# Kernel tuning notes

Hardware: AMD Instinct MI355X
Metric: run time of the kernel (lower is better)

The kernel has to match this reference:

```python
import jax, jax.numpy as jnp
import numpy as np

B, C, H, W = 4, 256, 48, 48
KD, NH, AR = 32, 8, 4
D = AR * KD            # 128, value dim per head
NHKD = NH * KD         # 256
DH = NH * D            # 1024
EPS = 1e-5


def _bn(y, g, b):
    # BN with fresh running stats (mean=0, var=1): y*g/sqrt(1+eps)+b, over channel dim
    s = g / jnp.sqrt(jnp.float32(1.0) + EPS)
    return y * s[None, :, None] + b[None, :, None]


def setup_inputs() -> dict:
    key = jax.random.key(0)
    ks = jax.random.split(key, 13)
    w = lambda k, sh: jax.random.normal(k, sh, jnp.float32) * 0.05
    g = lambda k, sh: 1.0 + jax.random.normal(k, sh, jnp.float32) * 0.05
    return {
        "x": jax.random.normal(ks[0], (B, C, H, W), jnp.float32),
        "wq": w(ks[1], (NHKD, C)), "gq": g(ks[2], (NHKD,)), "bq": w(ks[3], (NHKD,)),
        "wk": w(ks[4], (NHKD, C)), "gk": g(ks[5], (NHKD,)), "bk": w(ks[6], (NHKD,)),
        "wv": w(ks[7], (DH, C)),   "gv": g(ks[8], (DH,)),   "bv": w(ks[9], (DH,)),
        "wp": w(ks[10], (C, DH)),  "gp": g(ks[11], (C,)),   "bp": w(ks[12], (C,)),
    }


def reference(x, wq, gq, bq, wk, gk, bk, wv, gv, bv, wp, gp, bp):
    b, c, h, w = x.shape
    n = h * w
    xf = x.reshape(b, c, n)                                   # [B,C,N]
    # 1x1 conv == channel matmul, then BN
    q = _bn(jnp.einsum('oc,bcn->bon', wq, xf), gq, bq).reshape(b, NH, KD, n)
    k = _bn(jnp.einsum('oc,bcn->bon', wk, xf), gk, bk).reshape(b, NH, KD, n)
    v = _bn(jnp.einsum('oc,bcn->bon', wv, xf), gv, bv).reshape(b, NH, D, n)
    # NOTE: original forward does NOT apply self.scale
    attn = jax.nn.softmax(jnp.einsum('bhkn,bhkm->bhnm', q, k), axis=-1)  # [B,H,N,N]
    xx = jnp.einsum('bhnm,bhdm->bhdn', attn, v).reshape(b, DH, n)        # [B,DH,N]
    out = _bn(jnp.einsum('oc,bcn->bon', wp, jax.nn.relu(xx)), gp, bp)
    return out.reshape(b, c, h, w)
```

## Files before the change

### kernel.cpp

```cpp
#include <hip/hip_runtime.h>

#define BB 4
#define C 256
#define HW 2304
#define NH 8
#define KD 32
#define D 128
#define DH 1024
#define MQ 256

typedef unsigned short bf16u;
typedef __attribute__((ext_vector_type(8))) short short8;
typedef __attribute__((ext_vector_type(4))) short bfx4;
typedef __attribute__((ext_vector_type(4))) float f32x4;
typedef __attribute__((ext_vector_type(4))) unsigned ux4;
typedef __attribute__((ext_vector_type(2))) unsigned ux2;

union U8 { ux4 u; short8 s; };
union V8 { short8 s; bfx4 h[2]; };

__device__ __forceinline__ bf16u f2b(float f) {
    unsigned u = __float_as_uint(f);
    return (bf16u)((u + 0x7fffu + ((u >> 16) & 1u)) >> 16);
}
__device__ __forceinline__ unsigned pkb(float a, float b) {
    return __builtin_amdgcn_perm(__float_as_uint(b) + 0x8000u,
                                 __float_as_uint(a) + 0x8000u, 0x07060302u);
}

__device__ __forceinline__ void glds16(const bf16u* g, bf16u* l) {
    __builtin_amdgcn_global_load_lds(
        (const __attribute__((address_space(1))) unsigned int*)g,
        (__attribute__((address_space(3))) unsigned int*)l,
        16, 0, 0);
}

#define MFMA32 __builtin_amdgcn_mfma_f32_16x16x32_bf16

__global__ __launch_bounds__(256) void prep(
    const float* __restrict__ wq, const float* __restrict__ wk, const float* __restrict__ wv,
    const float* __restrict__ gq, const float* __restrict__ bq,
    const float* __restrict__ gk, const float* __restrict__ bk,
    const float* __restrict__ gv, const float* __restrict__ bv,
    bf16u* __restrict__ Wc, float* __restrict__ biasc)
{
    const float rs = rsqrtf(1.0f + 1e-5f);
    const float L2E = 1.4426950408889634f;
    const int t = threadIdx.x, blk = blockIdx.x;
    if (blk < 192) {
        const int idx = (blk*256 + t) * 8;
        const int row = idx >> 8;
        const float* src; float sc;
        if (idx < 65536)       { src = wq + idx;            sc = gq[row]*rs*L2E; }
        else if (idx < 131072) { src = wk + (idx - 65536);  sc = gk[row-256]*rs; }
        else                   { src = wv + (idx - 131072); sc = gv[row-512]*rs; }
        float4 a = *(const float4*)(src);
        float4 c = *(const float4*)(src + 4);
        ux4 v;
        v.x = pkb(a.x*sc, a.y*sc); v.y = pkb(a.z*sc, a.w*sc);
        v.z = pkb(c.x*sc, c.y*sc); v.w = pkb(c.z*sc, c.w*sc);
        *(ux4*)(Wc + idx) = v;
    } else {
        #pragma unroll
        for (int k = 0; k < 6; ++k) {
            const int r = k*256 + t;
            float v;
            if (r < 256)      v = bq[r] * L2E;
            else if (r < 512) v = bk[r - 256];
            else              v = bv[r - 512];
            biasc[r] = v;
        }
    }
}

__global__ __launch_bounds__(256) void xtrans(const float* __restrict__ x,
                                              bf16u* __restrict__ xT)
{
    const int c0 = blockIdx.x * 64, n0 = blockIdx.y * 64, b = blockIdx.z;
    const int t = threadIdx.x;
    __shared__ float tile[64][68];

    const float* xb = x + (size_t)b * C * HW;
    #pragma unroll
    for (int rr = 0; rr < 4; ++rr) {
        const int cl = rr*16 + (t >> 4);
        float4 v = *(const float4*)(xb + (size_t)(c0 + cl) * HW + n0 + (t & 15)*4);
        tile[cl][(t&15)*4+0] = v.x; tile[cl][(t&15)*4+1] = v.y;
        tile[cl][(t&15)*4+2] = v.z; tile[cl][(t&15)*4+3] = v.w;
    }
    __syncthreads();
    const int nl = t >> 2, ch = t & 3;
    short8 v0, v1;
    #pragma unroll
    for (int kk = 0; kk < 8; ++kk) v0[kk] = (short)f2b(tile[ch*16+kk][nl]);
    #pragma unroll
    for (int kk = 0; kk < 8; ++kk) v1[kk] = (short)f2b(tile[ch*16+8+kk][nl]);
    bf16u* dst = xT + ((size_t)b*HW + n0 + nl) * C + c0 + ch*16;
    *(short8*)(dst)     = v0;
    *(short8*)(dst + 8) = v1;
}

__global__ __launch_bounds__(256, 3) void qkv_gemm(
    const bf16u* __restrict__ Wc, const float* __restrict__ biasc,
    const bf16u* __restrict__ xT,
    bf16u* __restrict__ qT, bf16u* __restrict__ kT, bf16u* __restrict__ vO)
{
    const int mt = blockIdx.x, ntb = blockIdx.y, b = blockIdx.z;
    const int r0 = mt * 128, c0 = ntb * 128;
    const int t = threadIdx.x, w = t >> 6, l = t & 63;
    const int l15 = l & 15, q = l >> 4;
    const int wr = w >> 1, wc = w & 1;

    __shared__ bf16u smem[24576];

    const bf16u* xb = xT + (size_t)b * HW * C;

    const int sA0 = (w*2+0)*64 + l, sA1 = (w*2+1)*64 + l;
    const bf16u* gA0 = Wc + (size_t)(r0 + (sA0>>2)) * C + (sA0&3)*8;
    const bf16u* gA1 = Wc + (size_t)(r0 + (sA1>>2)) * C + (sA1&3)*8;
    const bf16u* gB0 = xb + (size_t)(c0 + (sA0>>2)) * C + (sA0&3)*8;
    const bf16u* gB1 = xb + (size_t)(c0 + (sA1>>2)) * C + (sA1&3)*8;

    f32x4 acc[4][4];
    #pragma unroll
    for (int i = 0; i < 4; ++i)
        #pragma unroll
        for (int j = 0; j < 4; ++j) { acc[i][j][0]=0.f; acc[i][j][1]=0.f; acc[i][j][2]=0.f; acc[i][j][3]=0.f; }

    auto stage = [&](int it2, int bb) {
        const int k0 = it2 * 32;
        bf16u* As = smem + bb*4096;
        bf16u* Bs = smem + 12288 + bb*4096;
        glds16(gA0 + k0, As + (w*2+0)*512);
        glds16(gA1 + k0, As + (w*2+1)*512);
        glds16(gB0 + k0, Bs + (w*2+0)*512);
        glds16(gB1 + k0, Bs + (w*2+1)*512);
    };

    const bool isV = (r0 >= 512);
    stage(0, 0); stage(1, 1);
    for (int it = 0; it < 8; ++it) {
        __syncthreads();
        if (it + 2 < 8) stage(it + 2, (it + 2) % 3);
        const bf16u* A = smem + (it % 3) * 4096;
        const bf16u* B = smem + 12288 + (it % 3) * 4096;
        short8 af[4], bf[4];
        #pragma unroll
        for (int i = 0; i < 4; ++i) af[i] = *(const short8*)(A + (wr*64 + i*16 + l15)*32 + q*8);
        #pragma unroll
        for (int j = 0; j < 4; ++j) bf[j] = *(const short8*)(B + (wc*64 + j*16 + l15)*32 + q*8);
        if (!isV) {
            #pragma unroll
            for (int i = 0; i < 4; ++i)
                #pragma unroll
                for (int j = 0; j < 4; ++j)
                    acc[i][j] = MFMA32(af[i], bf[j], acc[i][j], 0, 0, 0);
        } else {
            #pragma unroll
            for (int i = 0; i < 4; ++i)
                #pragma unroll
                for (int j = 0; j < 4; ++j)
                    acc[i][j] = MFMA32(bf[j], af[i], acc[i][j], 0, 0, 0);
        }
    }

    __syncthreads();
    bf16u* Od = smem + w * 4096;

    if (!isV) {
        float bC[4][4];
        #pragma unroll
        for (int i = 0; i < 4; ++i)
            #pragma unroll
            for (int r = 0; r < 4; ++r)
                bC[i][r] = biasc[r0 + wr*64 + i*16 + q*4 + r];
        #pragma unroll
        for (int i = 0; i < 4; ++i)
            #pragma unroll
            for (int j = 0; j < 4; ++j) {
                float y0 = acc[i][j][0] + bC[i][0];
                float y1 = acc[i][j][1] + bC[i][1];
                float y2 = acc[i][j][2] + bC[i][2];
                float y3 = acc[i][j][3] + bC[i][3];
                ux2 pk; pk.x = pkb(y0, y1); pk.y = pkb(y2, y3);
                const int row = j*16 + l15;
                const int ch  = (i*2 + (q >> 1)) ^ (l15 & 7);
                *(ux2*)(Od + row*64 + ch*8 + (q & 1)*4) = pk;
            }
        bf16u* dst = (r0 < 256) ? qT : kT;
        const int n = c0 + wc*64 + l;
        #pragma unroll
        for (int c = 0; c < 8; ++c) {
            short8 v = *(const short8*)(Od + l*64 + ((c ^ (l & 7)) * 8));
            const int ocg = (r0 & 255) + wr*64 + c*8;
            const int h = ocg >> 5, kd0 = ocg & 31;
            *(short8*)(dst + ((size_t)(b*NH + h) * HW + n) * KD + kd0) = v;
        }
    } else {
        float bC[4];
        #pragma unroll
        for (int i = 0; i < 4; ++i)
            bC[i] = biasc[r0 + wr*64 + i*16 + l15];
        #pragma unroll
        for (int i = 0; i < 4; ++i)
            #pragma unroll
            for (int j = 0; j < 4; ++j) {
                float y0 = acc[i][j][0] + bC[i];
                float y1 = acc[i][j][1] + bC[i];
                float y2 = acc[i][j][2] + bC[i];
                float y3 = acc[i][j][3] + bC[i];
                ux2 pk; pk.x = pkb(y0, y1); pk.y = pkb(y2, y3);
                const int row = i*16 + l15;
                const int ch  = (j*2 + (q >> 1)) ^ (l15 & 7);
                *(ux2*)(Od + row*64 + ch*8 + (q & 1)*4) = pk;
            }
        bf16u* dst = vO + (size_t)b * DH * HW;
        const int d = (r0 - 512) + wr*64 + l;
        #pragma unroll
        for (int c = 0; c < 8; ++c) {
            short8 v = *(const short8*)(Od + l*64 + ((c ^ (l & 7)) * 8));
            const int n = c0 + wc*64 + c*8;
            *(short8*)(dst + (size_t)d * HW + n) = v;
        }
    }
}

__global__ __launch_bounds__(256, 3) void attn_mfma(
    const bf16u* __restrict__ qT, const bf16u* __restrict__ kT,
    const bf16u* __restrict__ vg, bf16u* __restrict__ xg)
{
    const int nt = blockIdx.x, h = blockIdx.y, b = blockIdx.z;
    const int n0 = nt * 128;
    const int t = threadIdx.x;
    const int w = t >> 6, l = t & 63, l15 = l & 15, q = l >> 4;

    const bf16u* qTh = qT + (size_t)(b*NH + h) * HW * KD;
    const bf16u* kTh = kT + (size_t)(b*NH + h) * HW * KD;
    const bf16u* vh  = vg + ((size_t)b*DH + (size_t)h*D) * HW;

    __shared__ bf16u smem[20480];

    short8 qf0 = *(const short8*)(qTh + (size_t)(n0 + w*32 +      l15) * KD + q*8);
    short8 qf1 = *(const short8*)(qTh + (size_t)(n0 + w*32 + 16 + l15) * KD + q*8);

    f32x4 o[2][8];
    #pragma unroll
    for (int a = 0; a < 2; ++a)
        #pragma unroll
        for (int d = 0; d < 8; ++d) { o[a][d][0]=0.f; o[a][d][1]=0.f; o[a][d][2]=0.f; o[a][d][3]=0.f; }
    float psum0 = 0.f, psum1 = 0.f;
    const f32x4 zero = {0.f, 0.f, 0.f, 0.f};

    auto stage = [&](int m0, int bb) {
        bf16u* Ks = smem + bb*2048;
        bf16u* Vs = smem + 4096 + bb*8192;
        glds16(kTh + (size_t)m0*KD + (w*64 + l)*8, Ks + w*512);
        #pragma unroll
        for (int j = 0; j < 4; ++j) {
            const int s = (w*4 + j)*64 + l;
            const int d = s >> 3, c = s & 7, cg = c ^ (d & 7);
            glds16(vh + (size_t)d*HW + m0 + cg*8, Vs + (w*4 + j)*512);
        }
    };

    stage(0, 0);
    for (int mt = 0; mt < 36; ++mt) {
        __syncthreads();
        if (mt < 35) stage((mt+1)*64, (mt+1)&1);
        const bf16u* Ks = smem + (mt&1)*2048;
        const bf16u* Vs = smem + 4096 + (mt&1)*8192;

        f32x4 st0[4], st1[4];
        #pragma unroll
        for (int kt = 0; kt < 4; ++kt) {
            short8 kf = *(const short8*)(Ks + (kt*16 + l15)*KD + q*8);
            st0[kt] = MFMA32(kf, qf0, zero, 0, 0, 0);
            st1[kt] = MFMA32(kf, qf1, zero, 0, 0, 0);
        }

        unsigned dA0[4], dB0[4], dA1[4], dB1[4];
        #pragma unroll
        for (int kt = 0; kt < 4; ++kt) {
            float p0 = __builtin_amdgcn_exp2f(st0[kt][0]);
            float p1 = __builtin_amdgcn_exp2f(st0[kt][1]);
            float p2 = __builtin_amdgcn_exp2f(st0[kt][2]);
            float p3 = __builtin_amdgcn_exp2f(st0[kt][3]);
            psum0 += (p0 + p1) + (p2 + p3);
            dA0[kt] = pkb(p0, p1); dB0[kt] = pkb(p2, p3);
            float r0_ = __builtin_amdgcn_exp2f(st1[kt][0]);
            float r1_ = __builtin_amdgcn_exp2f(st1[kt][1]);
            float r2_ = __builtin_amdgcn_exp2f(st1[kt][2]);
            float r3_ = __builtin_amdgcn_exp2f(st1[kt][3]);
            psum1 += (r0_ + r1_) + (r2_ + r3_);
            dA1[kt] = pkb(r0_, r1_); dB1[kt] = pkb(r2_, r3_);
        }

        #pragma unroll
        for (int kh = 0; kh < 2; ++kh) {
            U8 u0, u1;
            u0.u[0] = dA0[kh*2];   u0.u[1] = dB0[kh*2];
            u0.u[2] = dA0[kh*2+1]; u0.u[3] = dB0[kh*2+1];
            u1.u[0] = dA1[kh*2];   u1.u[1] = dB1[kh*2];
            u1.u[2] = dA1[kh*2+1]; u1.u[3] = dB1[kh*2+1];
            const int clo = kh*4 + (q >> 1);
            const int chi = clo + 2;
            const int sub = (q & 1) * 4;
            #pragma unroll
            for (int dt = 0; dt < 8; ++dt) {
                const int d = dt*16 + l15;
                V8 vv;
                vv.h[0] = *(const bfx4*)(Vs + d*64 + ((clo ^ (d & 7)) * 8) + sub);
                vv.h[1] = *(const bfx4*)(Vs + d*64 + ((chi ^ (d & 7)) * 8) + sub);
                o[0][dt] = MFMA32(u0.s, vv.s, o[0][dt], 0, 0, 0);
                o[1][dt] = MFMA32(u1.s, vv.s, o[1][dt], 0, 0, 0);
            }
        }
    }

    psum0 += __shfl_xor(psum0, 16); psum0 += __shfl_xor(psum0, 32);
    psum1 += __shfl_xor(psum1, 16); psum1 += __shfl_xor(psum1, 32);
    float inv0[4], inv1[4];
    #pragma unroll
    for (int r = 0; r < 4; ++r) {
        inv0[r] = 1.0f / __shfl(psum0, q*4 + r);
        inv1[r] = 1.0f / __shfl(psum1, q*4 + r);
    }
    __syncthreads();
    bf16u* Od = smem + w * 4352;
    #pragma unroll
    for (int dt = 0; dt < 8; ++dt)
        #pragma unroll
        for (int r = 0; r < 4; ++r) {
            float v0 = fmaxf(o[0][dt][r] * inv0[r], 0.f);
            float v1 = fmaxf(o[1][dt][r] * inv1[r], 0.f);
            Od[(     q*4 + r)*136 + dt*16 + l15] = f2b(v0);
            Od[(16 + q*4 + r)*136 + dt*16 + l15] = f2b(v1);
        }
    bf16u* xb = xg + ((size_t)b*HW + n0 + w*32) * DH + h*D;
    #pragma unroll
    for (int rr = 0; rr < 2; ++rr) {
        const int row = rr*16 + (l >> 2), c = l & 3;
        #pragma unroll
        for (int kk = 0; kk < 4; ++kk)
            *(short8*)(xb + (size_t)row*DH + c*32 + kk*8) =
                *(const short8*)(Od + row*136 + c*32 + kk*8);
    }
}

__global__ __launch_bounds__(256, 3) void out_gemm(
    const float* __restrict__ wp, const float* __restrict__ gp, const float* __restrict__ bp,
    const bf16u* __restrict__ xx, float* __restrict__ out)
{
    const int mt = blockIdx.x, ntb = blockIdx.y, b = blockIdx.z;
    const int r0 = mt * 64, c0 = ntb * 64;
    const int t = threadIdx.x, w = t >> 6, l = t & 63;
    const int l15 = l & 15, q = l >> 4;
    const int wr = w >> 1, wc = w & 1;

    __shared__ bf16u smem[24576];

    const bf16u* xb = xx + (size_t)b * HW * DH;

    const int sA0 = t, sA1 = 256 + t;
    const float* gA0 = wp + (size_t)(r0 + (sA0>>3)) * DH + (sA0&7)*8;
    const float* gA1 = wp + (size_t)(r0 + (sA1>>3)) * DH + (sA1&7)*8;
    const int sB0 = w*128 + l, sB1 = w*128 + 64 + l;
    const bf16u* gB0 = xb + (size_t)(c0 + (sB0>>3)) * DH + (sB0&7)*8;
    const bf16u* gB1 = xb + (size_t)(c0 + (sB1>>3)) * DH + (sB1&7)*8;

    f32x4 acc[2][2];
    #pragma unroll
    for (int i = 0; i < 2; ++i)
        #pragma unroll
        for (int j = 0; j < 2; ++j) { acc[i][j][0]=0.f; acc[i][j][1]=0.f; acc[i][j][2]=0.f; acc[i][j][3]=0.f; }

    auto stage = [&](int it2, int bb) {
        const int k0 = it2 * 64;
        bf16u* As = smem + bb*4096;
        bf16u* Bs = smem + 12288 + bb*4096;
        glds16(gB0 + k0, Bs + (w*2+0)*512);
        glds16(gB1 + k0, Bs + (w*2+1)*512);
        #pragma unroll
        for (int jj = 0; jj < 2; ++jj) {
            const float* ga = jj ? gA1 : gA0;
            const int    s  = jj ? sA1 : sA0;
            float4 a = *(const float4*)(ga + k0);
            float4 c = *(const float4*)(ga + k0 + 4);
            ux4 v;
            v.x = pkb(a.x, a.y); v.y = pkb(a.z, a.w);
            v.z = pkb(c.x, c.y); v.w = pkb(c.z, c.w);
            *(ux4*)(As + s*8) = v;
        }
    };

    stage(0, 0); stage(1, 1);
    for (int it = 0; it < 16; ++it) {
        __syncthreads();
        if (it + 2 < 16) stage(it + 2, (it + 2) % 3);
        const bf16u* A = smem + (it % 3) * 4096;
        const bf16u* B = smem + 12288 + (it % 3) * 4096;
        #pragma unroll
        for (int kk = 0; kk < 2; ++kk) {
            short8 af[2], bf[2];
            #pragma unroll
            for (int i = 0; i < 2; ++i) af[i] = *(const short8*)(A + (wr*32 + i*16 + l15)*64 + kk*32 + q*8);
            #pragma unroll
            for (int j = 0; j < 2; ++j) bf[j] = *(const short8*)(B + (wc*32 + j*16 + l15)*64 + kk*32 + q*8);
            #pragma unroll
            for (int i = 0; i < 2; ++i)
                #pragma unroll
                for (int j = 0; j < 2; ++j)
                    acc[i][j] = MFMA32(af[i], bf[j], acc[i][j], 0, 0, 0);
        }
    }

    const float rs = rsqrtf(1.0f + 1e-5f);
    #pragma unroll
    for (int i = 0; i < 2; ++i)
        #pragma unroll
        for (int r = 0; r < 4; ++r) {
            const int oc = r0 + wr*32 + i*16 + q*4 + r;
            const float s = gp[oc]*rs, bi = bp[oc];
            #pragma unroll
            for (int j = 0; j < 2; ++j) {
                const int n = c0 + wc*32 + j*16 + l15;
                out[((size_t)b*C + oc)*HW + n] = acc[i][j][r]*s + bi;
            }
        }
}

extern "C" void kernel_launch(void* const* d_in, const int* in_sizes, int n_in,
                              void* d_out, int out_size, void* d_ws, size_t ws_size,
                              hipStream_t stream) {
    const float* x  = (const float*)d_in[0];
    const float* wq = (const float*)d_in[1];
    const float* gq = (const float*)d_in[2];
    const float* bq = (const float*)d_in[3];
    const float* wk = (const float*)d_in[4];
    const float* gk = (const float*)d_in[5];
    const float* bk = (const float*)d_in[6];
    const float* wv = (const float*)d_in[7];
    const float* gv = (const float*)d_in[8];
    const float* bv = (const float*)d_in[9];
    const float* wp = (const float*)d_in[10];
    const float* gp = (const float*)d_in[11];
    const float* bp = (const float*)d_in[12];
    float* out = (float*)d_out;

    bf16u* qw = (bf16u*)d_ws;
    bf16u* kw = qw + (size_t)BB * MQ * HW;
    bf16u* vw = kw + (size_t)BB * MQ * HW;
    bf16u* xw = vw + (size_t)BB * DH * HW;
    bf16u* xTb = xw;
    bf16u* Wc  = xw + (size_t)BB * MQ * HW;
    float* biasc = (float*)(Wc + 393216);

    hipLaunchKernelGGL(prep, dim3(193), dim3(256), 0, stream,
                       wq, wk, wv, gq, bq, gk, bk, gv, bv, Wc, biasc);
    hipLaunchKernelGGL(xtrans, dim3(4, 36, BB), dim3(256), 0, stream, x, xTb);
    hipLaunchKernelGGL(qkv_gemm, dim3(12, 18, BB), dim3(256), 0, stream,
                       Wc, biasc, xTb, qw, kw, vw);
    hipLaunchKernelGGL(attn_mfma, dim3(18, NH, BB), dim3(256), 0, stream,
                       qw, kw, vw, xw);
    hipLaunchKernelGGL(out_gemm, dim3(4, 36, BB), dim3(256), 0, stream,
                       wp, gp, bp, xw, out);
}
```

Measured before the change: 213.7 us.

## Pre-tile weights for direct LDS loads, permute V layout, shrink attention tiles

Weights for the QKV and output GEMMs are pre-converted into a tiled bf16 layout, so the GEMMs stage A with global_load_lds and no per-iteration fp32 conversion. The output projection's BN scale is folded into the weights by a new prep2 kernel. V is stored in a permuted order so attention reads full 16-byte V fragments. Attention now uses 64-row query tiles with K fragments held in registers and prefetched, doubling the grid and raising occupancy. The cost is an extra launch and heavier register/global traffic for K.

New measurement: 219.5 us. 2.7% more time.

```diff
diff --git a/kernel.cpp b/kernel.cpp
--- a/kernel.cpp
+++ b/kernel.cpp
@@ -42,7 +42,7 @@
     const float* __restrict__ gq, const float* __restrict__ bq,
     const float* __restrict__ gk, const float* __restrict__ bk,
     const float* __restrict__ gv, const float* __restrict__ bv,
-    bf16u* __restrict__ Wc, float* __restrict__ biasc)
+    bf16u* __restrict__ WcT, float* __restrict__ biasc)
 {
     const float rs = rsqrtf(1.0f + 1e-5f);
     const float L2E = 1.4426950408889634f;
@@ -50,20 +50,23 @@
     if (blk < 192) {
         const int idx = (blk*256 + t) * 8;
         const int row = idx >> 8;
+        const int k   = idx & 255;
         const float* src; float sc;
-        if (idx < 65536)       { src = wq + idx;            sc = gq[row]*rs*L2E; }
-        else if (idx < 131072) { src = wk + (idx - 65536);  sc = gk[row-256]*rs; }
-        else                   { src = wv + (idx - 131072); sc = gv[row-512]*rs; }
+        if (row < 256)      { src = wq + idx;            sc = gq[row]*rs*L2E; }
+        else if (row < 512) { src = wk + (idx - 65536);  sc = gk[row-256]*rs; }
+        else                { src = wv + (idx - 131072); sc = gv[row-512]*rs; }
         float4 a = *(const float4*)(src);
         float4 c = *(const float4*)(src + 4);
         ux4 v;
         v.x = pkb(a.x*sc, a.y*sc); v.y = pkb(a.z*sc, a.w*sc);
         v.z = pkb(c.x*sc, c.y*sc); v.w = pkb(c.z*sc, c.w*sc);
-        *(ux4*)(Wc + idx) = v;
+        const size_t dst = (size_t)((row>>7)*8 + (k>>5))*4096
+                         + (size_t)((row&127)*4 + ((k&31)>>3))*8;
+        *(ux4*)(WcT + dst) = v;
     } else {
         #pragma unroll
-        for (int k = 0; k < 6; ++k) {
-            const int r = k*256 + t;
+        for (int kk = 0; kk < 6; ++kk) {
+            const int r = kk*256 + t;
             float v;
             if (r < 256)      v = bq[r] * L2E;
             else if (r < 512) v = bk[r - 256];
@@ -101,7 +104,7 @@
 }
 
 __global__ __launch_bounds__(256, 3) void qkv_gemm(
-    const bf16u* __restrict__ Wc, const float* __restrict__ biasc,
+    const bf16u* __restrict__ WcT, const float* __restrict__ biasc,
     const bf16u* __restrict__ xT,
     bf16u* __restrict__ qT, bf16u* __restrict__ kT, bf16u* __restrict__ vO)
 {
@@ -115,9 +118,9 @@
 
     const bf16u* xb = xT + (size_t)b * HW * C;
 
-    const int sA0 = (w*2+0)*64 + l, sA1 = (w*2+1)*64 + l;
-    const bf16u* gA0 = Wc + (size_t)(r0 + (sA0>>2)) * C + (sA0&3)*8;
-    const bf16u* gA1 = Wc + (size_t)(r0 + (sA1>>2)) * C + (sA1&3)*8;
+    const int sA0 = w*128 + l, sA1 = w*128 + 64 + l;
+    const bf16u* gA0 = WcT + (size_t)mt*32768 + (size_t)sA0*8;
+    const bf16u* gA1 = WcT + (size_t)mt*32768 + (size_t)sA1*8;
     const bf16u* gB0 = xb + (size_t)(c0 + (sA0>>2)) * C + (sA0&3)*8;
     const bf16u* gB1 = xb + (size_t)(c0 + (sA1>>2)) * C + (sA1&3)*8;
 
@@ -128,13 +131,12 @@
         for (int j = 0; j < 4; ++j) { acc[i][j][0]=0.f; acc[i][j][1]=0.f; acc[i][j][2]=0.f; acc[i][j][3]=0.f; }
 
     auto stage = [&](int it2, int bb) {
-        const int k0 = it2 * 32;
         bf16u* As = smem + bb*4096;
         bf16u* Bs = smem + 12288 + bb*4096;
-        glds16(gA0 + k0, As + (w*2+0)*512);
-        glds16(gA1 + k0, As + (w*2+1)*512);
-        glds16(gB0 + k0, Bs + (w*2+0)*512);
-        glds16(gB1 + k0, Bs + (w*2+1)*512);
+        glds16(gA0 + it2*4096, As + sA0*8);
+        glds16(gA1 + it2*4096, As + sA1*8);
+        glds16(gB0 + it2*32,   Bs + sA0*8);
+        glds16(gB1 + it2*32,   Bs + sA1*8);
     };
 
     const bool isV = (r0 >= 512);
@@ -218,19 +220,25 @@
         const int d = (r0 - 512) + wr*64 + l;
         #pragma unroll
         for (int c = 0; c < 8; ++c) {
-            short8 v = *(const short8*)(Od + l*64 + ((c ^ (l & 7)) * 8));
-            const int n = c0 + wc*64 + c*8;
-            *(short8*)(dst + (size_t)d * HW + n) = v;
-        }
-    }
-}
-
-__global__ __launch_bounds__(256, 3) void attn_mfma(
+            V8 v; v.s = *(const short8*)(Od + l*64 + ((c ^ (l & 7)) * 8));
+            const int kh = c >> 2;
+            const int g0 = (2*c) & 7;
+            const int pos0 = kh*32 + (g0 & 3)*8 + (g0 >> 2)*4;
+            const int g1 = g0 + 1;
+            const int pos1 = kh*32 + (g1 & 3)*8 + (g1 >> 2)*4;
+            bf16u* dr = dst + (size_t)d * HW + c0 + wc*64;
+            *(bfx4*)(dr + pos0) = v.h[0];
+            *(bfx4*)(dr + pos1) = v.h[1];
+        }
+    }
+}
+
+__global__ __launch_bounds__(256, 4) void attn_mfma(
     const bf16u* __restrict__ qT, const bf16u* __restrict__ kT,
     const bf16u* __restrict__ vg, bf16u* __restrict__ xg)
 {
     const int nt = blockIdx.x, h = blockIdx.y, b = blockIdx.z;
-    const int n0 = nt * 128;
+    const int n0 = nt * 64;
     const int t = threadIdx.x;
     const int w = t >> 6, l = t & 63, l15 = l & 15, q = l >> 4;
 
@@ -238,23 +246,18 @@
     const bf16u* kTh = kT + (size_t)(b*NH + h) * HW * KD;
     const bf16u* vh  = vg + ((size_t)b*DH + (size_t)h*D) * HW;
 
-    __shared__ bf16u smem[20480];
-
-    short8 qf0 = *(const short8*)(qTh + (size_t)(n0 + w*32 +      l15) * KD + q*8);
-    short8 qf1 = *(const short8*)(qTh + (size_t)(n0 + w*32 + 16 + l15) * KD + q*8);
-
-    f32x4 o[2][8];
-    #pragma unroll
-    for (int a = 0; a < 2; ++a)
-        #pragma unroll
-        for (int d = 0; d < 8; ++d) { o[a][d][0]=0.f; o[a][d][1]=0.f; o[a][d][2]=0.f; o[a][d][3]=0.f; }
-    float psum0 = 0.f, psum1 = 0.f;
+    __shared__ bf16u smem[16384];
+
+    short8 qf = *(const short8*)(qTh + (size_t)(n0 + w*16 + l15) * KD + q*8);
+
+    f32x4 o[8];
+    #pragma unroll
+    for (int d = 0; d < 8; ++d) { o[d][0]=0.f; o[d][1]=0.f; o[d][2]=0.f; o[d][3]=0.f; }
+    float psum = 0.f;
     const f32x4 zero = {0.f, 0.f, 0.f, 0.f};
 
-    auto stage = [&](int m0, int bb) {
-        bf16u* Ks = smem + bb*2048;
-        bf16u* Vs = smem + 4096 + bb*8192;
-        glds16(kTh + (size_t)m0*KD + (w*64 + l)*8, Ks + w*512);
+    auto stageV = [&](int m0, int bb) {
+        bf16u* Vs = smem + bb*8192;
         #pragma unroll
         for (int j = 0; j < 4; ++j) {
             const int s = (w*4 + j)*64 + l;
@@ -263,92 +266,103 @@
         }
     };
 
-    stage(0, 0);
+    short8 kfc[4];
+    #pragma unroll
+    for (int kt = 0; kt < 4; ++kt)
+        kfc[kt] = *(const short8*)(kTh + (size_t)(kt*16 + l15) * KD + q*8);
+    stageV(0, 0);
+
     for (int mt = 0; mt < 36; ++mt) {
         __syncthreads();
-        if (mt < 35) stage((mt+1)*64, (mt+1)&1);
-        const bf16u* Ks = smem + (mt&1)*2048;
-        const bf16u* Vs = smem + 4096 + (mt&1)*8192;
-
-        f32x4 st0[4], st1[4];
+        if (mt < 35) stageV((mt+1)*64, (mt+1)&1);
+        const bf16u* Vs = smem + (mt&1)*8192;
+
+        short8 kfn[4];
+        if (mt < 35) {
+            #pragma unroll
+            for (int kt = 0; kt < 4; ++kt)
+                kfn[kt] = *(const short8*)(kTh + (size_t)((mt+1)*64 + kt*16 + l15) * KD + q*8);
+        }
+
+        f32x4 st[4];
+        #pragma unroll
+        for (int kt = 0; kt < 4; ++kt)
+            st[kt] = MFMA32(kfc[kt], qf, zero, 0, 0, 0);
+
+        unsigned dA[4], dB[4];
         #pragma unroll
         for (int kt = 0; kt < 4; ++kt) {
-            short8 kf = *(const short8*)(Ks + (kt*16 + l15)*KD + q*8);
-            st0[kt] = MFMA32(kf, qf0, zero, 0, 0, 0);
-            st1[kt] = MFMA32(kf, qf1, zero, 0, 0, 0);
-        }
-
-        unsigned dA0[4], dB0[4], dA1[4], dB1[4];
-        #pragma unroll
-        for (int kt = 0; kt < 4; ++kt) {
-            float p0 = __builtin_amdgcn_exp2f(st0[kt][0]);
-            float p1 = __builtin_amdgcn_exp2f(st0[kt][1]);
-            float p2 = __builtin_amdgcn_exp2f(st0[kt][2]);
-            float p3 = __builtin_amdgcn_exp2f(st0[kt][3]);
-            psum0 += (p0 + p1) + (p2 + p3);
-            dA0[kt] = pkb(p0, p1); dB0[kt] = pkb(p2, p3);
-            float r0_ = __builtin_amdgcn_exp2f(st1[kt][0]);
-            float r1_ = __builtin_amdgcn_exp2f(st1[kt][1]);
-            float r2_ = __builtin_amdgcn_exp2f(st1[kt][2]);
-            float r3_ = __builtin_amdgcn_exp2f(st1[kt][3]);
-            psum1 += (r0_ + r1_) + (r2_ + r3_);
-            dA1[kt] = pkb(r0_, r1_); dB1[kt] = pkb(r2_, r3_);
+            float p0 = __builtin_amdgcn_exp2f(st[kt][0]);
+            float p1 = __builtin_amdgcn_exp2f(st[kt][1]);
+            float p2 = __builtin_amdgcn_exp2f(st[kt][2]);
+            float p3 = __builtin_amdgcn_exp2f(st[kt][3]);
+            psum += (p0 + p1) + (p2 + p3);
+            dA[kt] = pkb(p0, p1); dB[kt] = pkb(p2, p3);
         }
 
         #pragma unroll
         for (int kh = 0; kh < 2; ++kh) {
-            U8 u0, u1;
-            u0.u[0] = dA0[kh*2];   u0.u[1] = dB0[kh*2];
-            u0.u[2] = dA0[kh*2+1]; u0.u[3] = dB0[kh*2+1];
-            u1.u[0] = dA1[kh*2];   u1.u[1] = dB1[kh*2];
-            u1.u[2] = dA1[kh*2+1]; u1.u[3] = dB1[kh*2+1];
-            const int clo = kh*4 + (q >> 1);
-            const int chi = clo + 2;
-            const int sub = (q & 1) * 4;
+            U8 u;
+            u.u[0] = dA[kh*2];   u.u[1] = dB[kh*2];
+            u.u[2] = dA[kh*2+1]; u.u[3] = dB[kh*2+1];
             #pragma unroll
             for (int dt = 0; dt < 8; ++dt) {
                 const int d = dt*16 + l15;
-                V8 vv;
-                vv.h[0] = *(const bfx4*)(Vs + d*64 + ((clo ^ (d & 7)) * 8) + sub);
-                vv.h[1] = *(const bfx4*)(Vs + d*64 + ((chi ^ (d & 7)) * 8) + sub);
-                o[0][dt] = MFMA32(u0.s, vv.s, o[0][dt], 0, 0, 0);
-                o[1][dt] = MFMA32(u1.s, vv.s, o[1][dt], 0, 0, 0);
+                short8 vf = *(const short8*)(Vs + d*64 + (((kh*4 + q) ^ (d & 7)) * 8));
+                o[dt] = MFMA32(u.s, vf, o[dt], 0, 0, 0);
             }
         }
-    }
-
-    psum0 += __shfl_xor(psum0, 16); psum0 += __shfl_xor(psum0, 32);
-    psum1 += __shfl_xor(psum1, 16); psum1 += __shfl_xor(psum1, 32);
-    float inv0[4], inv1[4];
-    #pragma unroll
-    for (int r = 0; r < 4; ++r) {
-        inv0[r] = 1.0f / __shfl(psum0, q*4 + r);
-        inv1[r] = 1.0f / __shfl(psum1, q*4 + r);
-    }
+
+        if (mt < 35) {
+            #pragma unroll
+            for (int kt = 0; kt < 4; ++kt) kfc[kt] = kfn[kt];
+        }
+    }
+
+    psum += __shfl_xor(psum, 16); psum += __shfl_xor(psum, 32);
+    float inv[4];
+    #pragma unroll
+    for (int r = 0; r < 4; ++r)
+        inv[r] = 1.0f / __shfl(psum, q*4 + r);
     __syncthreads();
-    bf16u* Od = smem + w * 4352;
+    bf16u* Od = smem + w * 2176;
     #pragma unroll
     for (int dt = 0; dt < 8; ++dt)
         #pragma unroll
         for (int r = 0; r < 4; ++r) {
-            float v0 = fmaxf(o[0][dt][r] * inv0[r], 0.f);
-            float v1 = fmaxf(o[1][dt][r] * inv1[r], 0.f);
-            Od[(     q*4 + r)*136 + dt*16 + l15] = f2b(v0);
-            Od[(16 + q*4 + r)*136 + dt*16 + l15] = f2b(v1);
-        }
-    bf16u* xb = xg + ((size_t)b*HW + n0 + w*32) * DH + h*D;
-    #pragma unroll
-    for (int rr = 0; rr < 2; ++rr) {
-        const int row = rr*16 + (l >> 2), c = l & 3;
-        #pragma unroll
-        for (int kk = 0; kk < 4; ++kk)
-            *(short8*)(xb + (size_t)row*DH + c*32 + kk*8) =
-                *(const short8*)(Od + row*136 + c*32 + kk*8);
-    }
+            float v = fmaxf(o[dt][r] * inv[r], 0.f);
+            Od[(q*4 + r)*136 + dt*16 + l15] = f2b(v);
+        }
+    bf16u* xb = xg + ((size_t)b*HW + n0 + w*16) * DH + h*D;
+    const int row = l >> 2, c = l & 3;
+    #pragma unroll
+    for (int kk = 0; kk < 4; ++kk)
+        *(short8*)(xb + (size_t)row*DH + c*32 + kk*8) =
+            *(const short8*)(Od + row*136 + c*32 + kk*8);
+}
+
+__global__ __launch_bounds__(256) void prep2(
+    const float* __restrict__ wp, const float* __restrict__ gp,
+    bf16u* __restrict__ WpT)
+{
+    const float rs = rsqrtf(1.0f + 1e-5f);
+    const int item = blockIdx.x*256 + threadIdx.x;
+    const int row = item >> 7;
+    const int k   = (item & 127) * 8;
+    const float sc = gp[row] * rs;
+    const float* src = wp + (size_t)row*DH + k;
+    float4 a = *(const float4*)(src);
+    float4 c = *(const float4*)(src + 4);
+    ux4 v;
+    v.x = pkb(a.x*sc, a.y*sc); v.y = pkb(a.z*sc, a.w*sc);
+    v.z = pkb(c.x*sc, c.y*sc); v.w = pkb(c.z*sc, c.w*sc);
+    const size_t dst = (size_t)((row>>6)*16 + (k>>6))*4096
+                     + (size_t)((row&63)*8 + ((k&63)>>3))*8;
+    *(ux4*)(WpT + dst) = v;
 }
 
 __global__ __launch_bounds__(256, 3) void out_gemm(
-    const float* __restrict__ wp, const float* __restrict__ gp, const float* __restrict__ bp,
+    const bf16u* __restrict__ WpT, const float* __restrict__ bp,
     const bf16u* __restrict__ xx, float* __restrict__ out)
 {
     const int mt = blockIdx.x, ntb = blockIdx.y, b = blockIdx.z;
@@ -362,8 +376,8 @@
     const bf16u* xb = xx + (size_t)b * HW * DH;
 
     const int sA0 = t, sA1 = 256 + t;
-    const float* gA0 = wp + (size_t)(r0 + (sA0>>3)) * DH + (sA0&7)*8;
-    const float* gA1 = wp + (size_t)(r0 + (sA1>>3)) * DH + (sA1&7)*8;
+    const bf16u* gA0 = WpT + (size_t)mt*65536 + (size_t)sA0*8;
+    const bf16u* gA1 = WpT + (size_t)mt*65536 + (size_t)sA1*8;
     const int sB0 = w*128 + l, sB1 = w*128 + 64 + l;
     const bf16u* gB0 = xb + (size_t)(c0 + (sB0>>3)) * DH + (sB0&7)*8;
     const bf16u* gB1 = xb + (size_t)(c0 + (sB1>>3)) * DH + (sB1&7)*8;
@@ -375,22 +389,12 @@
         for (int j = 0; j < 2; ++j) { acc[i][j][0]=0.f; acc[i][j][1]=0.f; acc[i][j][2]=0.f; acc[i][j][3]=0.f; }
 
     auto stage = [&](int it2, int bb) {
-        const int k0 = it2 * 64;
         bf16u* As = smem + bb*4096;
         bf16u* Bs = smem + 12288 + bb*4096;
-        glds16(gB0 + k0, Bs + (w*2+0)*512);
-        glds16(gB1 + k0, Bs + (w*2+1)*512);
-        #pragma unroll
-        for (int jj = 0; jj < 2; ++jj) {
-            const float* ga = jj ? gA1 : gA0;
-            const int    s  = jj ? sA1 : sA0;
-            float4 a = *(const float4*)(ga + k0);
-            float4 c = *(const float4*)(ga + k0 + 4);
-            ux4 v;
-            v.x = pkb(a.x, a.y); v.y = pkb(a.z, a.w);
-            v.z = pkb(c.x, c.y); v.w = pkb(c.z, c.w);
-            *(ux4*)(As + s*8) = v;
-        }
+        glds16(gA0 + it2*4096, As + sA0*8);
+        glds16(gA1 + it2*4096, As + sA1*8);
+        glds16(gB0 + it2*64,   Bs + sB0*8);
+        glds16(gB1 + it2*64,   Bs + sB1*8);
     };
 
     stage(0, 0); stage(1, 1);
@@ -414,17 +418,16 @@
         }
     }
 
-    const float rs = rsqrtf(1.0f + 1e-5f);
     #pragma unroll
     for (int i = 0; i < 2; ++i)
         #pragma unroll
         for (int r = 0; r < 4; ++r) {
             const int oc = r0 + wr*32 + i*16 + q*4 + r;
-            const float s = gp[oc]*rs, bi = bp[oc];
+            const float bi = bp[oc];
             #pragma unroll
             for (int j = 0; j < 2; ++j) {
                 const int n = c0 + wc*32 + j*16 + l15;
-                out[((size_t)b*C + oc)*HW + n] = acc[i][j][r]*s + bi;
+                out[((size_t)b*C + oc)*HW + n] = acc[i][j][r] + bi;
             }
         }
 }
@@ -452,16 +455,18 @@
     bf16u* vw = kw + (size_t)BB * MQ * HW;
     bf16u* xw = vw + (size_t)BB * DH * HW;
     bf16u* xTb = xw;
-    bf16u* Wc  = xw + (size_t)BB * MQ * HW;
-    float* biasc = (float*)(Wc + 393216);
+    bf16u* WcT = xw + (size_t)BB * MQ * HW;
+    float* biasc = (float*)(WcT + 393216);
+    bf16u* WpT = qw;
 
     hipLaunchKernelGGL(prep, dim3(193), dim3(256), 0, stream,
-                       wq, wk, wv, gq, bq, gk, bk, gv, bv, Wc, biasc);
+                       wq, wk, wv, gq, bq, gk, bk, gv, bv, WcT, biasc);
     hipLaunchKernelGGL(xtrans, dim3(4, 36, BB), dim3(256), 0, stream, x, xTb);
     hipLaunchKernelGGL(qkv_gemm, dim3(12, 18, BB), dim3(256), 0, stream,
-                       Wc, biasc, xTb, qw, kw, vw);
-    hipLaunchKernelGGL(attn_mfma, dim3(18, NH, BB), dim3(256), 0, stream,
+                       WcT, biasc, xTb, qw, kw, vw);
+    hipLaunchKernelGGL(attn_mfma, dim3(36, NH, BB), dim3(256), 0, stream,
                        qw, kw, vw, xw);
+    hipLaunchKernelGGL(prep2, dim3(128), dim3(256), 0, stream, wp, gp, WpT);
     hipLaunchKernelGGL(out_gemm, dim3(4, 36, BB), dim3(256), 0, stream,
-                       wp, gp, bp, xw, out);
-}
+                       WpT, bp, xw, out);
+}
```
